# Optimization experiments

Hardware: AMD Instinct MI355X
Metric: run time of the kernel (lower is better)

## Reference

```python
import jax, jax.numpy as jnp
import numpy as np

B, C_IN, H, W = 32, 512, 56, 56   # post-backbone feature map (resnet18, chan=64 -> 512 feats)
C_ENC = 64                         # topk_enc_chan
K = 256                            # topk_pxls_nb


def setup_inputs() -> dict:
    key = jax.random.key(0)
    k1, k2, k3 = jax.random.split(key, 3)
    return {
        "features": jax.random.normal(k1, (B, C_IN, H, W), jnp.float32),
        "conv_w": jax.random.normal(k2, (C_ENC, C_IN), jnp.float32) * 0.02,
        "conv_b": jax.random.normal(k3, (C_ENC,), jnp.float32) * 0.02,
    }


def reference(features, conv_w, conv_b):
    # 1x1 conv: [B,C_IN,H,W] -> [B,C_ENC,H,W]
    feats = jnp.einsum('bchw,oc->bohw', features, conv_w) + conv_b[None, :, None, None]
    b, c, h, w = feats.shape
    flat = feats.reshape(b, c, h * w)                      # [B,C,HW]
    # per-pixel squared L2 norm over channels
    norm = jnp.sum(flat * flat, axis=1)                    # [B,HW]
    _, idx = jax.lax.top_k(norm, K)                        # [B,K]
    abs_ = idx % w                                          # x coord
    ord_ = idx // w                                         # y coord
    # gather selected pixel features: mapToList equivalent -> [B,K,C]
    feat_list = jnp.take_along_axis(flat, idx[:, None, :], axis=2).transpose(0, 2, 1)
    x_out = feat_list.mean(axis=1)                         # [B,C]
    # scatter 1s into sparse attention map
    sw = jnp.zeros((b, h * w), feats.dtype).at[jnp.arange(b)[:, None], idx].set(1.0)
    sw = sw.reshape(b, 1, h, w)
    depth = jnp.zeros((b, K, 1), feats.dtype)
    points = jnp.concatenate(
        [abs_[..., None].astype(feats.dtype), ord_[..., None].astype(feats.dtype), depth, feat_list],
        axis=-1)                                           # [B,K,3+C]
    return (x_out, sw, points)
```

## Files before the change

kernel.cpp:

```cpp
#include <hip/hip_runtime.h>

#define B_     32
#define C_IN_  512
#define H_     56
#define W_     56
#define HW_    (H_ * W_)
#define C_ENC_ 64
#define K_     256
#define BHW_   (B_ * HW_)
#define PTS_ROW_ (3 + C_ENC_)

#define NCAND_ 320
#define SCH_   64
#define SNS_   (C_IN_ / SCH_)
#define GCH_   16
#define STILE_ 64
#define NTILE_ (NCAND_ / STILE_)
#define ECH_   64
#define ENS_   (C_IN_ / ECH_)

typedef float f32x4 __attribute__((ext_vector_type(4)));
typedef short bf16x8 __attribute__((ext_vector_type(8)));
typedef unsigned int uint;
typedef unsigned short ushort;
typedef unsigned long long ull;

__device__ __forceinline__ ushort f2bf(float f) {
    uint u = __float_as_uint(f);
    return (ushort)((u + 0x7FFFu + ((u >> 16) & 1u)) >> 16);
}

__device__ __forceinline__ void gload_lds16(const float* g, float* l) {
    __builtin_amdgcn_global_load_lds(
        (const __attribute__((address_space(1))) void*)g,
        (__attribute__((address_space(3))) void*)l, 16, 0, 0);
}

__global__ __launch_bounds__(256) void k_prep(
        const float* __restrict__ w, float* __restrict__ wt,
        ushort* __restrict__ wbf) {
    int i = blockIdx.x * 256 + threadIdx.x;
    if (i < C_ENC_ * C_IN_) {
        int o = i / C_IN_;
        int c = i % C_IN_;
        float v = w[i];
        wt[c * C_ENC_ + o] = v;
        wbf[i] = f2bf(v);
    }
}

__global__ __launch_bounds__(256) void k_screen(
        const float* __restrict__ F, const ushort* __restrict__ wbf,
        const float* __restrict__ bias, float* __restrict__ napprox) {
    __shared__ ushort xT[2][64][64];

    int t  = threadIdx.x;
    int l  = t & 63;
    int wv = t >> 6;
    int pb = blockIdx.x;
    int b  = pb / 49;
    int pixB = (pb % 49) * 64;

    int pxq = t & 15;
    int chg = t >> 4;
    const float* fb4 = F + (size_t)b * C_IN_ * HW_ + pixB + pxq * 4;

    int row = l & 15;
    int g   = l >> 4;
    int pxl = wv * 16 + (l & 15);
    int swR = (pxl & 7) << 3;

    f32x4 acc[4];
    #pragma unroll
    for (int ot = 0; ot < 4; ++ot) acc[ot] = (f32x4){0.f, 0.f, 0.f, 0.f};

    float4 xr4[4];

#define SCREEN_LOAD(S)                                                   \
    _Pragma("unroll") for (int u = 0; u < 4; ++u)                        \
        xr4[u] = *(const float4*)(fb4 +                                  \
                 (size_t)((S) * SCH_ + chg * 4 + u) * HW_);

#define SCREEN_WRITE(BUF)                                                \
    _Pragma("unroll") for (int i = 0; i < 4; ++i) {                      \
        int px = pxq * 4 + i;                                            \
        int sw = (px & 7) << 3;                                          \
        uint lo, hi;                                                     \
        asm volatile("v_cvt_pk_bf16_f32 %0, %1, %2" : "=v"(lo)           \
            : "v"(((const float*)&xr4[0])[i]),                           \
              "v"(((const float*)&xr4[1])[i]));                          \
        asm volatile("v_cvt_pk_bf16_f32 %0, %1, %2" : "=v"(hi)           \
            : "v"(((const float*)&xr4[2])[i]),                           \
              "v"(((const float*)&xr4[3])[i]));                          \
        uint2 pk; pk.x = lo; pk.y = hi;                                  \
        *(uint2*)&xT[BUF][px][(chg * 4) ^ sw] = pk;                      \
    }

    SCREEN_LOAD(0)
    SCREEN_WRITE(0)
    __syncthreads();

    for (int s = 0; s < SNS_; ++s) {
        if (s + 1 < SNS_) {
            SCREEN_LOAD(s + 1)
            __builtin_amdgcn_sched_barrier(0);
        }
        #pragma unroll
        for (int ks = 0; ks < 2; ++ks) {
            int cblk = (ks * 32 + g * 8) ^ swR;
            bf16x8 bfrag = *(const bf16x8*)&xT[s & 1][pxl][cblk];
            #pragma unroll
            for (int ot = 0; ot < 4; ++ot) {
                const ushort* ap = wbf + (size_t)(ot * 16 + row) * C_IN_
                                       + s * SCH_ + ks * 32 + g * 8;
                bf16x8 afrag = *(const bf16x8*)ap;
                acc[ot] = __builtin_amdgcn_mfma_f32_16x16x32_bf16(
                        afrag, bfrag, acc[ot], 0, 0, 0);
            }
        }
        if (s + 1 < SNS_) {
            asm volatile("s_waitcnt vmcnt(0)" ::: "memory");
            SCREEN_WRITE((s + 1) & 1)
        }
        __syncthreads();
    }

    float partial = 0.0f;
    #pragma unroll
    for (int ot = 0; ot < 4; ++ot) {
        float4 b4 = *(const float4*)(bias + ot * 16 + g * 4);
        float v0 = acc[ot][0] + b4.x;
        float v1 = acc[ot][1] + b4.y;
        float v2 = acc[ot][2] + b4.z;
        float v3 = acc[ot][3] + b4.w;
        partial = fmaf(v0, v0, partial);
        partial = fmaf(v1, v1, partial);
        partial = fmaf(v2, v2, partial);
        partial = fmaf(v3, v3, partial);
    }
    partial += __shfl_xor(partial, 16);
    partial += __shfl_xor(partial, 32);
    if (l < 16)
        napprox[b * HW_ + pixB + wv * 16 + l] = partial;
}

__global__ __launch_bounds__(512) void k_sel(
        const float* __restrict__ napprox, uint* __restrict__ cand) {
    __shared__ uint keys[HW_];
    __shared__ uint hist[256];
    __shared__ uint s_prefix, s_need, s_cnt;

    int b = blockIdx.x;
    int t = threadIdx.x;
    const float* nb = napprox + b * HW_;

    for (int i = t; i < HW_; i += 512) keys[i] = __float_as_uint(nb[i]);
    if (t == 0) { s_prefix = 0u; s_need = (uint)NCAND_; s_cnt = 0u; }

    for (int r = 0; r < 4; ++r) {
        if (t < 256) hist[t] = 0u;
        __syncthreads();
        uint pfx = s_prefix;
        int shift = 24 - 8 * r;
        for (int i = t; i < HW_; i += 512) {
            uint k = keys[i];
            bool ok = (r == 0) || ((k >> (32 - 8 * r)) == pfx);
            if (ok) atomicAdd(&hist[(k >> shift) & 0xFFu], 1u);
        }
        __syncthreads();
        if (t < 64) {
            uint h0 = hist[4 * t + 0], h1 = hist[4 * t + 1];
            uint h2 = hist[4 * t + 2], h3 = hist[4 * t + 3];
            uint suf = h0 + h1 + h2 + h3;
            #pragma unroll
            for (int off = 1; off < 64; off <<= 1) {
                uint v = __shfl_down(suf, off);
                suf += (t + off < 64) ? v : 0u;
            }
            uint g0 = suf, g1 = suf - h0, g2 = g1 - h1, g3 = g2 - h2,
                 g4 = g3 - h3;
            uint need = s_need;
            if (g0 >= need && g1 < need) { s_prefix = (pfx << 8) | (4u*t+0u); s_need = need - g1; }
            if (g1 >= need && g2 < need) { s_prefix = (pfx << 8) | (4u*t+1u); s_need = need - g2; }
            if (g2 >= need && g3 < need) { s_prefix = (pfx << 8) | (4u*t+2u); s_need = need - g3; }
            if (g3 >= need && g4 < need) { s_prefix = (pfx << 8) | (4u*t+3u); s_need = need - g4; }
        }
        __syncthreads();
    }
    uint T = s_prefix;

    for (int i = t; i < HW_; i += 512) {
        if (keys[i] >= T) {
            uint pos = atomicAdd(&s_cnt, 1u);
            if (pos < NCAND_) cand[b * NCAND_ + pos] = (uint)i;
        }
    }
    __syncthreads();
    for (int i = s_cnt + t; i < NCAND_; i += 512)
        cand[b * NCAND_ + i] = 0xFFFFFFFFu;
}

__global__ __launch_bounds__(512) void k_gather(
        const float* __restrict__ F, const uint* __restrict__ cand,
        float* __restrict__ xg) {
    __shared__ float rowf[2][HW_];
    __shared__ uint scand[NCAND_];

    int t = threadIdx.x;
    int bid = blockIdx.x;
    int b = bid >> 5;
    int c0 = (bid & 31) * GCH_;

    for (int i = t; i < NCAND_; i += 512) scand[i] = cand[b * NCAND_ + i];

    const float* src = F + ((size_t)b * C_IN_ + c0) * HW_;
    int wvb = (t >> 6) * 256;
    int ln4 = (t & 63) * 4;

#define G_STAGE(BUF, CI)                                                 \
    {                                                                    \
        const float* sp = src + (size_t)(CI) * HW_;                      \
        gload_lds16(sp + wvb + ln4, &rowf[BUF][wvb]);                    \
        if (2048 + wvb + ln4 < HW_)                                      \
            gload_lds16(sp + 2048 + wvb + ln4, &rowf[BUF][2048 + wvb]);  \
    }

    G_STAGE(0, 0)
    asm volatile("s_waitcnt vmcnt(0)" ::: "memory");
    __syncthreads();

    for (int i = 0; i < GCH_; ++i) {
        if (i + 1 < GCH_) G_STAGE((i + 1) & 1, i + 1)
        if (t < NCAND_) {
            uint p = scand[t];
            xg[((size_t)b * C_IN_ + c0 + i) * NCAND_ + t] =
                (p == 0xFFFFFFFFu) ? 0.0f : rowf[i & 1][p];
        }
        asm volatile("s_waitcnt vmcnt(0)" ::: "memory");
        __syncthreads();
    }
#undef G_STAGE
}

__global__ __launch_bounds__(256) void k_exact2(
        const float* __restrict__ xg, const float* __restrict__ wt,
        const float* __restrict__ bias, float* __restrict__ cand_feats) {
    __shared__ float xb[2][ECH_][STILE_];

    int bid = blockIdx.x;
    int b = bid / NTILE_;
    int tile = bid - b * NTILE_;
    int t = threadIdx.x;
    int l = t & 63;
    int g = __builtin_amdgcn_readfirstlane(t >> 6);

    const float* gs = xg + ((size_t)b * C_IN_) * NCAND_ + tile * STILE_
                         + (size_t)(l >> 4) * NCAND_ + (l & 15) * 4;
    const float* wg = wt + g * 16;

    float acc[16];
    #pragma unroll
    for (int o = 0; o < 16; ++o) acc[o] = bias[g * 16 + o];

    #pragma unroll
    for (int u = 0; u < 4; ++u)
        gload_lds16(gs + (size_t)(g * 16 + u * 4) * NCAND_,
                    &xb[0][g * 16 + u * 4][0]);
    asm volatile("s_waitcnt vmcnt(0)" ::: "memory");
    __syncthreads();

    for (int s = 0; s < ENS_; ++s) {
        if (s + 1 < ENS_) {
            int cn = (s + 1) * ECH_ + g * 16;
            float* dst = &xb[(s + 1) & 1][g * 16][0];
            #pragma unroll
            for (int u = 0; u < 4; ++u)
                gload_lds16(gs + (size_t)(cn + u * 4) * NCAND_,
                            dst + u * 4 * STILE_);
        }
        {
            int cb = s * ECH_;
            #pragma unroll 8
            for (int cl = 0; cl < ECH_; ++cl) {
                float x = xb[s & 1][cl][l];
                #pragma unroll
                for (int o = 0; o < 16; ++o)
                    acc[o] = fmaf(x, wg[(cb + cl) * C_ENC_ + o], acc[o]);
            }
        }
        asm volatile("s_waitcnt vmcnt(0)" ::: "memory");
        __syncthreads();
    }

    float* fo = cand_feats + ((size_t)b * NCAND_ + tile * STILE_ + l) * C_ENC_
              + g * 16;
    #pragma unroll
    for (int o = 0; o < 16; ++o) fo[o] = acc[o];
}

__global__ __launch_bounds__(512) void k_topk2(
        const float* __restrict__ cand_feats, const uint* __restrict__ cand,
        uint* __restrict__ topk_pix, uint* __restrict__ topk_slot,
        float* __restrict__ sw_out) {
    __shared__ ull sortbuf[512];
    __shared__ unsigned char flags[HW_];

    int b = blockIdx.x;
    int t = threadIdx.x;

    for (int i = t; i < HW_; i += 512) flags[i] = 0;

    ull key = ~0ULL;
    if (t < NCAND_) {
        uint p = cand[b * NCAND_ + t];
        if (p != 0xFFFFFFFFu) {
            const float* fr = cand_feats + ((size_t)b * NCAND_ + t) * C_ENC_;
            float nrm = 0.0f;
            for (int o = 0; o < C_ENC_; ++o) nrm = fmaf(fr[o], fr[o], nrm);
            uint nb = __float_as_uint(nrm);
            key = ((ull)(~nb) << 32) | ((ull)(p << 9)) | (ull)(uint)t;
        }
    }
    sortbuf[t] = key;
    __syncthreads();

    for (int kk = 2; kk <= 512; kk <<= 1) {
        for (int j = kk >> 1; j > 0; j >>= 1) {
            int ixj = t ^ j;
            if (ixj > t) {
                ull a = sortbuf[t], c = sortbuf[ixj];
                bool up = ((t & kk) == 0);
                if ((a > c) == up) { sortbuf[t] = c; sortbuf[ixj] = a; }
            }
            __syncthreads();
        }
    }

    if (t < K_) {
        ull e = sortbuf[t];
        uint low = (uint)e;
        uint pix = low >> 9;
        uint sl  = low & 511u;
        topk_pix[b * K_ + t]  = pix;
        topk_slot[b * K_ + t] = sl;
        flags[pix] = 1;
    }
    __syncthreads();

    float* swb = sw_out + b * HW_;
    for (int i = t; i < HW_; i += 512)
        swb[i] = flags[i] ? 1.0f : 0.0f;
}

__global__ __launch_bounds__(64) void k_points(
        const float* __restrict__ cand_feats, const uint* __restrict__ topk_pix,
        const uint* __restrict__ topk_slot, float* __restrict__ points) {
    int bk = blockIdx.x;
    int b = bk >> 8;
    int o = threadIdx.x;
    uint p  = topk_pix[bk];
    uint sl = topk_slot[bk];

    float v = cand_feats[((size_t)b * NCAND_ + sl) * C_ENC_ + o];
    float* row = points + (size_t)bk * PTS_ROW_;
    row[3 + o] = v;
    if (o == 0) {
        row[0] = (float)(p % W_);
        row[1] = (float)(p / W_);
        row[2] = 0.0f;
    }
}

__global__ __launch_bounds__(64) void k_xout(
        const float* __restrict__ cand_feats, const uint* __restrict__ topk_slot,
        float* __restrict__ xout) {
    __shared__ uint sslot[K_];
    int b = blockIdx.x;
    int t = threadIdx.x;
    for (int r = t; r < K_; r += 64) sslot[r] = topk_slot[b * K_ + r];
    __syncthreads();

    float s = 0.0f;
    #pragma unroll 8
    for (int k = 0; k < K_; ++k)
        s += cand_feats[((size_t)b * NCAND_ + sslot[k]) * C_ENC_ + t];
    xout[b * C_ENC_ + t] = s * (1.0f / K_);
}

extern "C" void kernel_launch(void* const* d_in, const int* in_sizes, int n_in,
                              void* d_out, int out_size, void* d_ws, size_t ws_size,
                              hipStream_t stream) {
    const float* F    = (const float*)d_in[0];
    const float* w    = (const float*)d_in[1];
    const float* bias = (const float*)d_in[2];

    float* out    = (float*)d_out;
    float* xout   = out;
    float* sw     = out + B_ * C_ENC_;
    float* points = sw + BHW_;

    float* wt         = (float*)d_ws;
    float* napprox    = wt + C_IN_ * C_ENC_;
    float* xg         = napprox + BHW_;
    float* cand_feats = xg + (size_t)B_ * C_IN_ * NCAND_;
    uint*  cand       = (uint*)(cand_feats + (size_t)B_ * NCAND_ * C_ENC_);
    uint*  topk_pix   = cand + B_ * NCAND_;
    uint*  topk_slot  = topk_pix + B_ * K_;
    ushort* wbf       = (ushort*)(topk_slot + B_ * K_);

    k_prep   <<<128, 256, 0, stream>>>(w, wt, wbf);
    k_screen <<<BHW_ / 64, 256, 0, stream>>>(F, wbf, bias, napprox);
    k_sel    <<<B_, 512, 0, stream>>>(napprox, cand);
    k_gather <<<B_ * (C_IN_ / GCH_), 512, 0, stream>>>(F, cand, xg);
    k_exact2 <<<B_ * NTILE_, 256, 0, stream>>>(xg, wt, bias, cand_feats);
    k_topk2  <<<B_, 512, 0, stream>>>(cand_feats, cand, topk_pix, topk_slot, sw);
    k_points <<<B_ * K_, 64, 0, stream>>>(cand_feats, topk_pix, topk_slot, points);
    k_xout   <<<B_, 64, 0, stream>>>(cand_feats, topk_slot, xout);
}
```

Baseline: 176.1 us.

## Deepen screen-kernel prefetch and fuse topk, points and xout kernels

Restructures the screening GEMM loop to double-bank its register prefetch, loading input tiles two stages ahead and preloading weight fragments before each MFMA block so global latency overlaps compute. Separately fuses the top-k sort, points write and mean reduction into one kernel that keeps the selected indices in shared memory. This removes two launches and the global round trip for the top-k index arrays. The fused kernel writes points rows with one thread per row, which may coalesce worse, and the deeper prefetch raises register use.

```diff
diff --git a/kernel.cpp b/kernel.cpp
--- a/kernel.cpp
+++ b/kernel.cpp
@@ -74,54 +74,63 @@
     #pragma unroll
     for (int ot = 0; ot < 4; ++ot) acc[ot] = (f32x4){0.f, 0.f, 0.f, 0.f};
 
-    float4 xr4[4];
-
-#define SCREEN_LOAD(S)                                                   \
+    float4 xrA[4], xrB[4];
+    bf16x8 af[2][4];
+
+#define SCREEN_LOAD(BANK, S)                                             \
     _Pragma("unroll") for (int u = 0; u < 4; ++u)                        \
-        xr4[u] = *(const float4*)(fb4 +                                  \
+        BANK[u] = *(const float4*)(fb4 +                                 \
                  (size_t)((S) * SCH_ + chg * 4 + u) * HW_);
 
-#define SCREEN_WRITE(BUF)                                                \
+#define SCREEN_WRITE(BANK, BUF)                                          \
     _Pragma("unroll") for (int i = 0; i < 4; ++i) {                      \
         int px = pxq * 4 + i;                                            \
         int sw = (px & 7) << 3;                                          \
         uint lo, hi;                                                     \
         asm volatile("v_cvt_pk_bf16_f32 %0, %1, %2" : "=v"(lo)           \
-            : "v"(((const float*)&xr4[0])[i]),                           \
-              "v"(((const float*)&xr4[1])[i]));                          \
+            : "v"(((const float*)&BANK[0])[i]),                          \
+              "v"(((const float*)&BANK[1])[i]));                         \
         asm volatile("v_cvt_pk_bf16_f32 %0, %1, %2" : "=v"(hi)           \
-            : "v"(((const float*)&xr4[2])[i]),                           \
-              "v"(((const float*)&xr4[3])[i]));                          \
+            : "v"(((const float*)&BANK[2])[i]),                          \
+              "v"(((const float*)&BANK[3])[i]));                         \
         uint2 pk; pk.x = lo; pk.y = hi;                                  \
         *(uint2*)&xT[BUF][px][(chg * 4) ^ sw] = pk;                      \
     }
 
-    SCREEN_LOAD(0)
-    SCREEN_WRITE(0)
-    __syncthreads();
-
-    for (int s = 0; s < SNS_; ++s) {
-        if (s + 1 < SNS_) {
-            SCREEN_LOAD(s + 1)
-            __builtin_amdgcn_sched_barrier(0);
-        }
-        #pragma unroll
-        for (int ks = 0; ks < 2; ++ks) {
-            int cblk = (ks * 32 + g * 8) ^ swR;
-            bf16x8 bfrag = *(const bf16x8*)&xT[s & 1][pxl][cblk];
-            #pragma unroll
-            for (int ot = 0; ot < 4; ++ot) {
-                const ushort* ap = wbf + (size_t)(ot * 16 + row) * C_IN_
-                                       + s * SCH_ + ks * 32 + g * 8;
-                bf16x8 afrag = *(const bf16x8*)ap;
-                acc[ot] = __builtin_amdgcn_mfma_f32_16x16x32_bf16(
-                        afrag, bfrag, acc[ot], 0, 0, 0);
-            }
-        }
-        if (s + 1 < SNS_) {
-            asm volatile("s_waitcnt vmcnt(0)" ::: "memory");
-            SCREEN_WRITE((s + 1) & 1)
-        }
+#define AFRAG_LOAD(S)                                                    \
+    _Pragma("unroll") for (int ks = 0; ks < 2; ++ks)                     \
+        _Pragma("unroll") for (int ot = 0; ot < 4; ++ot)                 \
+            af[ks][ot] = *(const bf16x8*)(wbf +                          \
+                (size_t)(ot * 16 + row) * C_IN_ + (S) * SCH_ + ks * 32 + g * 8);
+
+#define SCREEN_MFMA(S)                                                   \
+    _Pragma("unroll") for (int ks = 0; ks < 2; ++ks) {                   \
+        int cblk = (ks * 32 + g * 8) ^ swR;                              \
+        bf16x8 bfrag = *(const bf16x8*)&xT[(S) & 1][pxl][cblk];          \
+        _Pragma("unroll") for (int ot = 0; ot < 4; ++ot)                 \
+            acc[ot] = __builtin_amdgcn_mfma_f32_16x16x32_bf16(           \
+                    af[ks][ot], bfrag, acc[ot], 0, 0, 0);                \
+    }
+
+    SCREEN_LOAD(xrA, 0)
+    SCREEN_LOAD(xrB, 1)
+    SCREEN_WRITE(xrA, 0)
+    __syncthreads();
+
+    for (int sp = 0; sp < SNS_; sp += 2) {
+        AFRAG_LOAD(sp)
+        __builtin_amdgcn_sched_barrier(0);
+        if (sp + 2 < SNS_) { SCREEN_LOAD(xrA, sp + 2) }
+        __builtin_amdgcn_sched_barrier(0);
+        SCREEN_MFMA(sp)
+        SCREEN_WRITE(xrB, 1)
+        __syncthreads();
+        AFRAG_LOAD(sp + 1)
+        __builtin_amdgcn_sched_barrier(0);
+        if (sp + 3 < SNS_) { SCREEN_LOAD(xrB, sp + 3) }
+        __builtin_amdgcn_sched_barrier(0);
+        SCREEN_MFMA(sp + 1)
+        if (sp + 2 < SNS_) { SCREEN_WRITE(xrA, 0) }
         __syncthreads();
     }
 
@@ -298,12 +307,14 @@
     for (int o = 0; o < 16; ++o) fo[o] = acc[o];
 }
 
-__global__ __launch_bounds__(512) void k_topk2(
+__global__ __launch_bounds__(512) void k_final(
         const float* __restrict__ cand_feats, const uint* __restrict__ cand,
-        uint* __restrict__ topk_pix, uint* __restrict__ topk_slot,
-        float* __restrict__ sw_out) {
+        float* __restrict__ sw_out, float* __restrict__ points,
+        float* __restrict__ xout) {
     __shared__ ull sortbuf[512];
     __shared__ unsigned char flags[HW_];
+    __shared__ uint spix[K_];
+    __shared__ uint sslot[K_];
 
     int b = blockIdx.x;
     int t = threadIdx.x;
@@ -341,8 +352,8 @@
         uint low = (uint)e;
         uint pix = low >> 9;
         uint sl  = low & 511u;
-        topk_pix[b * K_ + t]  = pix;
-        topk_slot[b * K_ + t] = sl;
+        spix[t] = pix;
+        sslot[t] = sl;
         flags[pix] = 1;
     }
     __syncthreads();
@@ -350,41 +361,26 @@
     float* swb = sw_out + b * HW_;
     for (int i = t; i < HW_; i += 512)
         swb[i] = flags[i] ? 1.0f : 0.0f;
-}
-
-__global__ __launch_bounds__(64) void k_points(
-        const float* __restrict__ cand_feats, const uint* __restrict__ topk_pix,
-        const uint* __restrict__ topk_slot, float* __restrict__ points) {
-    int bk = blockIdx.x;
-    int b = bk >> 8;
-    int o = threadIdx.x;
-    uint p  = topk_pix[bk];
-    uint sl = topk_slot[bk];
-
-    float v = cand_feats[((size_t)b * NCAND_ + sl) * C_ENC_ + o];
-    float* row = points + (size_t)bk * PTS_ROW_;
-    row[3 + o] = v;
-    if (o == 0) {
+
+    if (t < K_) {
+        uint p  = spix[t];
+        uint sl = sslot[t];
+        const float* fr = cand_feats + ((size_t)b * NCAND_ + sl) * C_ENC_;
+        float* row = points + (size_t)(b * K_ + t) * PTS_ROW_;
         row[0] = (float)(p % W_);
         row[1] = (float)(p / W_);
         row[2] = 0.0f;
-    }
-}
-
-__global__ __launch_bounds__(64) void k_xout(
-        const float* __restrict__ cand_feats, const uint* __restrict__ topk_slot,
-        float* __restrict__ xout) {
-    __shared__ uint sslot[K_];
-    int b = blockIdx.x;
-    int t = threadIdx.x;
-    for (int r = t; r < K_; r += 64) sslot[r] = topk_slot[b * K_ + r];
-    __syncthreads();
-
-    float s = 0.0f;
-    #pragma unroll 8
-    for (int k = 0; k < K_; ++k)
-        s += cand_feats[((size_t)b * NCAND_ + sslot[k]) * C_ENC_ + t];
-    xout[b * C_ENC_ + t] = s * (1.0f / K_);
+        #pragma unroll 8
+        for (int o = 0; o < C_ENC_; ++o) row[3 + o] = fr[o];
+    }
+
+    if (t < C_ENC_) {
+        float s = 0.0f;
+        #pragma unroll 8
+        for (int k = 0; k < K_; ++k)
+            s += cand_feats[((size_t)b * NCAND_ + sslot[k]) * C_ENC_ + t];
+        xout[b * C_ENC_ + t] = s * (1.0f / K_);
+    }
 }
 
 extern "C" void kernel_launch(void* const* d_in, const int* in_sizes, int n_in,
@@ -404,16 +400,12 @@
     float* xg         = napprox + BHW_;
     float* cand_feats = xg + (size_t)B_ * C_IN_ * NCAND_;
     uint*  cand       = (uint*)(cand_feats + (size_t)B_ * NCAND_ * C_ENC_);
-    uint*  topk_pix   = cand + B_ * NCAND_;
-    uint*  topk_slot  = topk_pix + B_ * K_;
-    ushort* wbf       = (ushort*)(topk_slot + B_ * K_);
+    ushort* wbf       = (ushort*)(cand + B_ * NCAND_);
 
     k_prep   <<<128, 256, 0, stream>>>(w, wt, wbf);
     k_screen <<<BHW_ / 64, 256, 0, stream>>>(F, wbf, bias, napprox);
     k_sel    <<<B_, 512, 0, stream>>>(napprox, cand);
     k_gather <<<B_ * (C_IN_ / GCH_), 512, 0, stream>>>(F, cand, xg);
     k_exact2 <<<B_ * NTILE_, 256, 0, stream>>>(xg, wt, bias, cand_feats);
-    k_topk2  <<<B_, 512, 0, stream>>>(cand_feats, cand, topk_pix, topk_slot, sw);
-    k_points <<<B_ * K_, 64, 0, stream>>>(cand_feats, topk_pix, topk_slot, points);
-    k_xout   <<<B_, 64, 0, stream>>>(cand_feats, topk_slot, xout);
-}
+    k_final  <<<B_, 512, 0, stream>>>(cand_feats, cand, sw, points, xout);
+}
```

Result: no change. 175.3 us (-0.5%).
